# Optimization experiments

Measured on AMD Instinct MI355X. Metric: run time of the kernel, lower is better.

The kernel has to match this reference:

```python
import jax, jax.numpy as jnp
import numpy as np

NOISE_STD = 0.01  # noise_std init arg


def setup_inputs() -> dict:
    key = jax.random.key(0)
    k1, k2, k3, k4, k5 = jax.random.split(key, 5)
    B, C, H, W = 32, 256, 56, 56
    x = jax.random.normal(k1, (B, C, H, W), dtype=jnp.float32)
    H_real = jax.random.normal(k2, (B, C, C), dtype=jnp.float32)
    H_imag = jax.random.normal(k3, (B, C, C), dtype=jnp.float32)
    noise_real = jax.random.normal(k4, (B, C, H, W), dtype=jnp.float32)
    noise_imag = jax.random.normal(k5, (B, C, H, W), dtype=jnp.float32)
    return {"x": x, "H_real": H_real, "H_imag": H_imag,
            "noise_real": noise_real, "noise_imag": noise_imag}


def reference(x, H_real, H_imag, noise_real, noise_imag):
    # x: (B,C,H,W) real. Per-batch complex MIMO channel Hc = (Hr + i*Hi)/sqrt(2*C).
    # Since x has zero imaginary part, y = Hc @ x splits into two real GEMMs.
    C = x.shape[1]
    scale = 1.0 / jnp.sqrt(jnp.asarray(2.0 * C, dtype=x.dtype))
    yr = jnp.einsum('bij,bjhw->bihw', H_real, x) * scale + noise_real * NOISE_STD
    yi = jnp.einsum('bij,bjhw->bihw', H_imag, x) * scale + noise_imag * NOISE_STD
    # output_mode == 'magnitude' -> |y|
    return jnp.sqrt(yr * yr + yi * yi)
```

## Files before the change

### kernel.cpp

```cpp
#include <hip/hip_runtime.h>
#include <hip/hip_bf16.h>
#include <math.h>


#define NBATCH 32
#define NC 256
#define NP 3136
#define BM 128
#define BN 64
#define BK 32
#define NBN 49
#define NKI 8

typedef __attribute__((ext_vector_type(8))) short short8;
typedef __attribute__((ext_vector_type(4))) float f32x4;

static __device__ __forceinline__ void gload16(const void* g, void* l) {
  __builtin_amdgcn_global_load_lds(
      (const __attribute__((address_space(1))) void*)g,
      (__attribute__((address_space(3))) void*)l, 16, 0, 0);
}

static __device__ __forceinline__ unsigned short bfr(float f) {
  __hip_bfloat16 h = __float2bfloat16(f);
  return *reinterpret_cast<unsigned short*>(&h);
}

__global__ __launch_bounds__(256)
void perm_h_kernel(const float* __restrict__ hr, const float* __restrict__ hi,
                   unsigned short* __restrict__ ws)
{
  const int blk   = blockIdx.x;
  const int kt    = blk & 7;
  const int b2m   = blk >> 3;
  const int plane = threadIdx.x >> 7;
  const int row   = threadIdx.x & 127;
  const int b     = b2m >> 1;
  const int bm    = b2m & 1;

  const float* src = (plane ? hi : hr)
      + ((size_t)b * NC + bm * 128 + row) * NC + kt * 32;
  unsigned short* dst = ws + ((size_t)(b2m * 8 + kt) * 2 + plane) * 4096 + row * 8;

  #pragma unroll
  for (int fq = 0; fq < 4; ++fq) {
    const float4 v0 = *reinterpret_cast<const float4*>(src + fq * 8);
    const float4 v1 = *reinterpret_cast<const float4*>(src + fq * 8 + 4);
    union { uint4 v; unsigned short u[8]; } o;
    o.u[0] = bfr(v0.x); o.u[1] = bfr(v0.y); o.u[2] = bfr(v0.z); o.u[3] = bfr(v0.w);
    o.u[4] = bfr(v1.x); o.u[5] = bfr(v1.y); o.u[6] = bfr(v1.z); o.u[7] = bfr(v1.w);
    *reinterpret_cast<uint4*>(dst + fq * 1024) = o.v;
  }
}

template<int PRE>
__global__ __launch_bounds__(512, 4)
void rayleigh_main(const float* __restrict__ xg,
                   const float* __restrict__ Hrg,
                   const float* __restrict__ Hig,
                   const unsigned short* __restrict__ Hperm,
                   const float* __restrict__ nrg,
                   const float* __restrict__ nig,
                   float* __restrict__ outg)
{
  __shared__ float x_lds[2][BK * BN];
  __shared__ unsigned short hr_lds[2][4096];
  __shared__ unsigned short hi_lds[2][4096];

  const int raw = blockIdx.x;
  const int v   = (raw & 7) * 392 + (raw >> 3);
  const int b   = v / 98;
  const int r2  = v - b * 98;
  const int bm  = r2 / 49;
  const int bn  = r2 - bm * 49;

  const int tid  = threadIdx.x;
  const int lane = tid & 63;
  const int wave = tid >> 6;
  const int wm   = wave >> 2;
  const int wn   = wave & 3;
  const int fr   = lane & 15;
  const int fq   = lane >> 4;

  const float* xsrc = xg + (size_t)b * NC * NP + (size_t)bn * BN;
  const size_t hrowbase = (size_t)b * NC + bm * BM;
  const size_t hpbase = (size_t)((b * 2 + bm) * 8);

  auto stage = [&](int t, int buf) {
    {
      const int C16 = wave * 64 + lane;
      const int k   = C16 >> 4;
      const int cp  = C16 & 15;
      const int fqk = k >> 3;
      const int cl  = cp ^ (((fqk & 1) << 2) | (fqk >> 1));
      const float* src = xsrc + (size_t)(t * BK + k) * NP + cl * 4;
      gload16(src, (char*)x_lds[buf] + wave * 1024);
    }
    if constexpr (PRE) {
      #pragma unroll
      for (int i = 0; i < 2; ++i) {
        const int c     = wave * 2 + i;
        const int plane = c >> 3;
        const int fqc   = (c >> 1) & 3;
        const int half  = c & 1;
        unsigned short* hl = plane ? hi_lds[buf] : hr_lds[buf];
        const unsigned short* src = Hperm
            + ((hpbase + t) * 2 + plane) * 4096
            + fqc * 1024 + (half * 64 + lane) * 8;
        gload16(src, (char*)hl + fqc * 2048 + half * 1024);
      }
    }
  };

  f32x4 accR[4], accI[4];
  #pragma unroll
  for (int m = 0; m < 4; ++m) {
    accR[m] = (f32x4){0.f, 0.f, 0.f, 0.f};
    accI[m] = (f32x4){0.f, 0.f, 0.f, 0.f};
  }
  float nrv[4][4], niv[4][4];

  const size_t obase = ((size_t)b * NC + bm * BM + wm * 64 + fq * 4) * NP
                     + (size_t)bn * BN + wn * 16 + fr;
  const int xork = ((fq & 1) << 6) | ((fq >> 1) << 4);
  const int pcol = ((wn * 16 + fr) << 2) ^ xork;

  stage(0, 0);

  #pragma unroll
  for (int t = 0; t < NKI; ++t) {
    __syncthreads();
    if (t + 1 < NKI) stage(t + 1, (t + 1) & 1);

    {
      const int m = t >> 1, rb = (t & 1) * 2;
      #pragma unroll
      for (int r = 0; r < 2; ++r) {
        const size_t idx = obase + (size_t)(m * 16 + rb + r) * NP;
        nrv[m][rb + r] = __builtin_nontemporal_load(nrg + idx);
        niv[m][rb + r] = __builtin_nontemporal_load(nig + idx);
      }
    }

    const char* xbuf = (const char*)x_lds[t & 1];
    union { short8 s; unsigned short u[8]; } u;
    #pragma unroll
    for (int j = 0; j < 8; ++j) {
      const float f = *reinterpret_cast<const float*>(xbuf + ((fq * 8 + j) << 8) + pcol);
      u.u[j] = bfr(f);
    }
    const short8 xb = u.s;

    #pragma unroll
    for (int m = 0; m < 4; ++m) {
      const int row = wm * 64 + m * 16 + fr;
      short8 ar, ai;
      if constexpr (PRE) {
        ar = *reinterpret_cast<const short8*>(&hr_lds[t & 1][fq * 1024 + row * 8]);
        ai = *reinterpret_cast<const short8*>(&hi_lds[t & 1][fq * 1024 + row * 8]);
      } else {
        const float* p1 = Hrg + (hrowbase + row) * NC + t * BK + fq * 8;
        const float* p2 = Hig + (hrowbase + row) * NC + t * BK + fq * 8;
        const float4 v0 = *reinterpret_cast<const float4*>(p1);
        const float4 v1 = *reinterpret_cast<const float4*>(p1 + 4);
        const float4 w0 = *reinterpret_cast<const float4*>(p2);
        const float4 w1 = *reinterpret_cast<const float4*>(p2 + 4);
        union { short8 s; unsigned short uu[8]; } a1, a2;
        a1.uu[0] = bfr(v0.x); a1.uu[1] = bfr(v0.y); a1.uu[2] = bfr(v0.z); a1.uu[3] = bfr(v0.w);
        a1.uu[4] = bfr(v1.x); a1.uu[5] = bfr(v1.y); a1.uu[6] = bfr(v1.z); a1.uu[7] = bfr(v1.w);
        a2.uu[0] = bfr(w0.x); a2.uu[1] = bfr(w0.y); a2.uu[2] = bfr(w0.z); a2.uu[3] = bfr(w0.w);
        a2.uu[4] = bfr(w1.x); a2.uu[5] = bfr(w1.y); a2.uu[6] = bfr(w1.z); a2.uu[7] = bfr(w1.w);
        ar = a1.s; ai = a2.s;
      }
      accR[m] = __builtin_amdgcn_mfma_f32_16x16x32_bf16(ar, xb, accR[m], 0, 0, 0);
      accI[m] = __builtin_amdgcn_mfma_f32_16x16x32_bf16(ai, xb, accI[m], 0, 0, 0);
    }
  }

  const float scale = 0.04419417382415922f;
  const float nstd  = 0.01f;
  #pragma unroll
  for (int m = 0; m < 4; ++m)
    #pragma unroll
    for (int r = 0; r < 4; ++r) {
      const size_t idx = obase + (size_t)(m * 16 + r) * NP;
      const float yr = accR[m][r] * scale + nrv[m][r] * nstd;
      const float yi = accI[m][r] * scale + niv[m][r] * nstd;
      outg[idx] = sqrtf(yr * yr + yi * yi);
    }
}

extern "C" void kernel_launch(void* const* d_in, const int* in_sizes, int n_in,
                              void* d_out, int out_size, void* d_ws, size_t ws_size,
                              hipStream_t stream) {
  const float* x  = (const float*)d_in[0];
  const float* Hr = (const float*)d_in[1];
  const float* Hi = (const float*)d_in[2];
  const float* nr = (const float*)d_in[3];
  const float* ni = (const float*)d_in[4];
  float* out = (float*)d_out;

  const size_t HN = (size_t)NBATCH * NC * NC;

  if (ws_size >= HN * 2 * sizeof(unsigned short)) {
    unsigned short* hperm = (unsigned short*)d_ws;
    hipLaunchKernelGGL(perm_h_kernel, dim3(512), dim3(256), 0, stream, Hr, Hi, hperm);
    hipLaunchKernelGGL((rayleigh_main<1>), dim3(NBATCH * 2 * NBN), dim3(512), 0, stream,
                       x, Hr, Hi, hperm, nr, ni, out);
  } else {
    hipLaunchKernelGGL((rayleigh_main<0>), dim3(NBATCH * 2 * NBN), dim3(512), 0, stream,
                       x, Hr, Hi, (const unsigned short*)nullptr, nr, ni, out);
  }
}
```

Measured before the change: 107.2 us.

## Swap MFMA operands for float4 epilogue, defer noise loads, raise occupancy hint

```diff
diff --git a/kernel.cpp b/kernel.cpp
--- a/kernel.cpp
+++ b/kernel.cpp
@@ -54,7 +54,7 @@
 }
 
 template<int PRE>
-__global__ __launch_bounds__(512, 4)
+__global__ __launch_bounds__(512, 6)
 void rayleigh_main(const float* __restrict__ xg,
                    const float* __restrict__ Hrg,
                    const float* __restrict__ Hig,
@@ -84,7 +84,7 @@
 
   const float* xsrc = xg + (size_t)b * NC * NP + (size_t)bn * BN;
   const size_t hrowbase = (size_t)b * NC + bm * BM;
-  const size_t hpbase = (size_t)((b * 2 + bm) * 8);
+  const size_t hpbase   = (size_t)((b * 2 + bm) * 8);
 
   auto stage = [&](int t, int buf) {
     {
@@ -118,10 +118,7 @@
     accR[m] = (f32x4){0.f, 0.f, 0.f, 0.f};
     accI[m] = (f32x4){0.f, 0.f, 0.f, 0.f};
   }
-  float nrv[4][4], niv[4][4];
-
-  const size_t obase = ((size_t)b * NC + bm * BM + wm * 64 + fq * 4) * NP
-                     + (size_t)bn * BN + wn * 16 + fr;
+
   const int xork = ((fq & 1) << 6) | ((fq >> 1) << 4);
   const int pcol = ((wn * 16 + fr) << 2) ^ xork;
 
@@ -131,16 +128,6 @@
   for (int t = 0; t < NKI; ++t) {
     __syncthreads();
     if (t + 1 < NKI) stage(t + 1, (t + 1) & 1);
-
-    {
-      const int m = t >> 1, rb = (t & 1) * 2;
-      #pragma unroll
-      for (int r = 0; r < 2; ++r) {
-        const size_t idx = obase + (size_t)(m * 16 + rb + r) * NP;
-        nrv[m][rb + r] = __builtin_nontemporal_load(nrg + idx);
-        niv[m][rb + r] = __builtin_nontemporal_load(nig + idx);
-      }
-    }
 
     const char* xbuf = (const char*)x_lds[t & 1];
     union { short8 s; unsigned short u[8]; } u;
@@ -159,8 +146,8 @@
         ar = *reinterpret_cast<const short8*>(&hr_lds[t & 1][fq * 1024 + row * 8]);
         ai = *reinterpret_cast<const short8*>(&hi_lds[t & 1][fq * 1024 + row * 8]);
       } else {
-        const float* p1 = Hrg + (hrowbase + row) * NC + t * BK + fq * 8;
-        const float* p2 = Hig + (hrowbase + row) * NC + t * BK + fq * 8;
+        const float* p1 = Hrg + (hrowbase + row) * NC + t * 32 + fq * 8;
+        const float* p2 = Hig + (hrowbase + row) * NC + t * 32 + fq * 8;
         const float4 v0 = *reinterpret_cast<const float4*>(p1);
         const float4 v1 = *reinterpret_cast<const float4*>(p1 + 4);
         const float4 w0 = *reinterpret_cast<const float4*>(p2);
@@ -172,22 +159,43 @@
         a2.uu[4] = bfr(w1.x); a2.uu[5] = bfr(w1.y); a2.uu[6] = bfr(w1.z); a2.uu[7] = bfr(w1.w);
         ar = a1.s; ai = a2.s;
       }
-      accR[m] = __builtin_amdgcn_mfma_f32_16x16x32_bf16(ar, xb, accR[m], 0, 0, 0);
-      accI[m] = __builtin_amdgcn_mfma_f32_16x16x32_bf16(ai, xb, accI[m], 0, 0, 0);
+      accR[m] = __builtin_amdgcn_mfma_f32_16x16x32_bf16(xb, ar, accR[m], 0, 0, 0);
+      accI[m] = __builtin_amdgcn_mfma_f32_16x16x32_bf16(xb, ai, accI[m], 0, 0, 0);
     }
   }
 
   const float scale = 0.04419417382415922f;
   const float nstd  = 0.01f;
-  #pragma unroll
-  for (int m = 0; m < 4; ++m)
-    #pragma unroll
-    for (int r = 0; r < 4; ++r) {
-      const size_t idx = obase + (size_t)(m * 16 + r) * NP;
-      const float yr = accR[m][r] * scale + nrv[m][r] * nstd;
-      const float yi = accI[m][r] * scale + niv[m][r] * nstd;
-      outg[idx] = sqrtf(yr * yr + yi * yi);
-    }
+  const size_t obase = ((size_t)b * NC + bm * BM + wm * 64 + fr) * NP
+                     + (size_t)bn * BN + wn * 16 + fq * 4;
+  #pragma unroll
+  for (int m = 0; m < 4; ++m) {
+    const size_t idx = obase + (size_t)(m * 16) * NP;
+    const float4 nr4 = *reinterpret_cast<const float4*>(nrg + idx);
+    const float4 ni4 = *reinterpret_cast<const float4*>(nig + idx);
+    float4 o;
+    {
+      const float yr = accR[m][0] * scale + nr4.x * nstd;
+      const float yi = accI[m][0] * scale + ni4.x * nstd;
+      o.x = sqrtf(yr * yr + yi * yi);
+    }
+    {
+      const float yr = accR[m][1] * scale + nr4.y * nstd;
+      const float yi = accI[m][1] * scale + ni4.y * nstd;
+      o.y = sqrtf(yr * yr + yi * yi);
+    }
+    {
+      const float yr = accR[m][2] * scale + nr4.z * nstd;
+      const float yi = accI[m][2] * scale + ni4.z * nstd;
+      o.z = sqrtf(yr * yr + yi * yi);
+    }
+    {
+      const float yr = accR[m][3] * scale + nr4.w * nstd;
+      const float yi = accI[m][3] * scale + ni4.w * nstd;
+      o.w = sqrtf(yr * yr + yi * yi);
+    }
+    *reinterpret_cast<float4*>(outg + idx) = o;
+  }
 }
 
 extern "C" void kernel_launch(void* const* d_in, const int* in_sizes, int n_in,
```

New measurement: 116.4 us. 1.09x slower.
